# Optimization experiments

Hardware: AMD Instinct MI355X
Metric: run time of the kernel (lower is better)

## Reference

```python
import jax, jax.numpy as jnp
import numpy as np

T, N, L, H, C, V = 64, 1024, 128, 512, 64, 64
S = 1 + 1 + H + (L + 1) + L  # pack layout: a(1), v(1), h(H), a_probs(L+1), p(L)


def setup_inputs() -> dict:
    key = jax.random.key(0)
    ks = jax.random.split(key, 16)

    def w(k, shape, fan):
        return jax.random.normal(k, shape, jnp.float32) / np.sqrt(fan)

    return {
        "condition": jax.random.normal(ks[0], (T, N, C), jnp.float32),
        "rnn_hxs": jnp.zeros((N, S), jnp.float32),  # all-zero => new episode
        "emb": w(ks[3], (V, H), H),
        "W0": w(ks[4], (H, C + H), C + H), "b0": jnp.zeros((H,), jnp.float32),
        "W1": w(ks[5], (H, H), H), "b1": jnp.zeros((H,), jnp.float32),
        "W2": w(ks[6], (H, H), H), "b2": jnp.zeros((H,), jnp.float32),
        "W_ih": w(ks[7], (3 * H, H), H), "b_ih": jnp.zeros((3 * H,), jnp.float32),
        "W_hh": w(ks[8], (3 * H, H), H), "b_hh": jnp.zeros((3 * H,), jnp.float32),
        "Wc": w(ks[9], (1, H), H), "bc": jnp.zeros((1,), jnp.float32),
        "Wa": w(ks[10], (4, H), H), "ba": jnp.zeros((4,), jnp.float32),
        "lines": jax.random.randint(ks[1], (N, L), 0, V),
        "actions": jax.random.randint(ks[2], (T, N), 0, L + 1),
    }


def _forward(condition, rnn_hxs, emb, W0, b0, W1, b1, W2, b2,
             W_ih, W_hh, b_ih, b_hh, Wc, bc, Wa, ba, lines, actions):
    M = emb[lines]  # [N, L, H] line embeddings (memory)
    # parse hidden in RecurrentState field order a(1), v(1), h(H), a_probs(L+1), p(L)
    h0 = rnn_hxs[:, 2:2 + H]
    p0 = rnn_hxs[:, 2 + H + (L + 1):]
    new_ep = jnp.all(rnn_hxs == 0, axis=-1)
    p0 = p0.at[:, 0].set(jnp.where(new_ep, 1.0, p0[:, 0]))

    def step(carry, xs):
        h, p = carry
        cond_t, a_t = xs
        # attention readout over memory
        r = jnp.einsum("nl,nlh->nh", p, M)
        # f: MLP on concat(condition, readout)
        x = jnp.concatenate([cond_t, r], axis=-1)
        x = jax.nn.relu(x @ W0.T + b0)
        x = jax.nn.relu(x @ W1.T + b1)
        x = jax.nn.relu(x @ W2.T + b2)
        # torch GRUCell math
        gi = x @ W_ih.T + b_ih
        gh = h @ W_hh.T + b_hh
        i_r, i_z, i_n = jnp.split(gi, 3, axis=-1)
        h_r, h_z, h_n = jnp.split(gh, 3, axis=-1)
        rg = jax.nn.sigmoid(i_r + h_r)
        z = jax.nn.sigmoid(i_z + h_z)
        n = jnp.tanh(i_n + rg * h_n)
        h = (1.0 - z) * n + z * h
        # actor -> 3 shift weights + no-op gate
        k = h @ Wa.T + ba
        l = jax.nn.softmax(k[:, :3], axis=-1)
        no_op = jax.nn.sigmoid(k[:, 3:4])
        # batch_conv1d: per-sample cross-correlation, kernel 3, padding 2 -> len L+2,
        # fold boundary mass inward, then slice [1:-1] -> len L
        xp = jnp.pad(p, ((0, 0), (2, 2)))
        y = (xp[:, 0:L + 2] * l[:, 0:1]
             + xp[:, 1:L + 3] * l[:, 1:2]
             + xp[:, 2:L + 4] * l[:, 2:3])
        y = y.at[:, 1].add(y[:, 0])
        y = y.at[:, L].add(y[:, L + 1])
        conv_p = y[:, 1:L + 1]
        probs = jnp.concatenate([conv_p * (1.0 - no_op), no_op], axis=-1)
        probs = probs / probs.sum(-1, keepdims=True)
        # pointer update (actions supplied non-negative => no sampling branch)
        new = a_t < L
        a = a_t * new.astype(a_t.dtype)
        newf = new.astype(p.dtype)[:, None]
        p = jax.nn.one_hot(a, L, dtype=p.dtype) * newf + p * (1.0 - newf)
        v = h @ Wc.T + bc
        out = jnp.concatenate(
            [a_t.astype(jnp.float32)[:, None], v, h, probs, p], axis=-1)
        return (h, p), out

    _, hx = jax.lax.scan(step, (h0, p0), (condition, actions))
    return hx  # [T, N, S]


def reference(condition, rnn_hxs, emb, W0, b0, W1, b1, W2, b2,
              W_ih, W_hh, b_ih, b_hh, Wc, bc, Wa, ba, lines, actions):
    hx = _forward(condition, rnn_hxs, emb, W0, b0, W1, b1, W2, b2,
                  W_ih, W_hh, b_ih, b_hh, Wc, bc, Wa, ba, lines, actions)
    return hx, hx[-1:]
```

## Files before the change

kernel.cpp:

```cpp
#include <hip/hip_runtime.h>
#include <hip/hip_bf16.h>
#include <stdint.h>

#define T_ 64
#define N_ 1024
#define L_ 128
#define H_ 512
#define C_ 64
#define S_ 771
#define TN_ (T_*N_)

typedef unsigned short u16;
typedef unsigned int u32;
typedef float f32x4 __attribute__((ext_vector_type(4)));
typedef __bf16 bf16x8 __attribute__((ext_vector_type(8)));
typedef u16 u16x8 __attribute__((ext_vector_type(8)));

#define WAITVM(n) do { asm volatile("s_waitcnt vmcnt(" #n ")" ::: "memory"); \
                       __builtin_amdgcn_sched_barrier(0); } while (0)

__device__ __forceinline__ u16 f2bf(float f) {
  u32 u = __float_as_uint(f);
  u32 r = (u + 0x7FFFu + ((u >> 16) & 1u)) >> 16;
  return (u16)r;
}
__device__ __forceinline__ float bf2f(u16 u) {
  return __uint_as_float(((u32)u) << 16);
}
__device__ __forceinline__ void gload16(const void* g, void* l) {
  __builtin_amdgcn_global_load_lds((const __attribute__((address_space(1))) u32*)g,
                                   (__attribute__((address_space(3))) u32*)l, 16, 0, 0);
}
__device__ __forceinline__ float sigm(float x) { return 1.0f / (1.0f + __expf(-x)); }

__device__ __forceinline__ bf16x8 load_cc(const u16* p) {
  bf16x8 v;
  asm volatile("global_load_dwordx4 %0, %1, off sc0 sc1" : "=v"(v) : "v"(p) : "memory");
  return v;
}
__device__ __forceinline__ void store_cc_d2(u16* p, uint2 val) {
  asm volatile("global_store_dwordx2 %0, %1, off sc0 sc1" :: "v"(p), "v"(val) : "memory");
}
__device__ __forceinline__ float gi_get(uint2 u, int v) {
  u32 w = (v < 2) ? u.x : u.y;
  u16 h = (v & 1) ? (u16)(w >> 16) : (u16)(w & 0xffffu);
  return bf2f(h);
}

__global__ void cast_f32_bf16(const float* __restrict__ src, u16* __restrict__ dst, int n) {
  int i = blockIdx.x * 256 + threadIdx.x;
  if (i < n) dst[i] = f2bf(src[i]);
}

__global__ void qscan(const float* __restrict__ hxs, const int* __restrict__ actions,
                      int* __restrict__ qpre, int* __restrict__ qpost) {
  int n = blockIdx.x * 256 + threadIdx.x;
  if (n >= N_) return;
  bool nz = false;
  for (int s = 0; s < S_; ++s) nz |= (hxs[(size_t)n * S_ + s] != 0.0f);
  int q = 0;
  if (nz) {
    float best = -3.4e38f;
    for (int l = 0; l < L_; ++l) {
      float v = hxs[(size_t)n * S_ + 2 + H_ + (L_ + 1) + l];
      if (v > best) { best = v; q = l; }
    }
  }
  for (int t = 0; t < T_; ++t) {
    qpre[t * N_ + n] = q;
    int a = actions[t * N_ + n];
    if (a < L_) q = a;
    qpost[t * N_ + n] = q;
  }
}

__global__ void hbf_init(const float* __restrict__ hxs, u16* __restrict__ hsave0) {
  int i = blockIdx.x * 256 + threadIdx.x;
  if (i >= N_ * H_) return;
  int n = i >> 9, j = i & 511;
  hsave0[i] = f2bf(hxs[(size_t)n * S_ + 2 + j]);
}

__global__ void build_abuf(const float* __restrict__ cond, const float* __restrict__ emb,
                           const int* __restrict__ lines, const int* __restrict__ qpre,
                           u16* __restrict__ abuf) {
  int row = blockIdx.x * 4 + (threadIdx.x >> 6);
  int lane = threadIdx.x & 63;
  int n = row & (N_ - 1);
  int q = qpre[row];
  int line = lines[n * L_ + q];
  abuf[(size_t)row * 576 + lane] = f2bf(cond[(size_t)row * 64 + lane]);
  const float* er = emb + (size_t)line * H_;
  u16* ar = abuf + (size_t)row * 576 + 64;
  for (int j = lane; j < H_; j += 64) ar[j] = f2bf(er[j]);
}

#define BM 128
#define BN 128
#define BK 64
__global__ __launch_bounds__(256) void gemm_nt(
    const u16* __restrict__ A, int lda,
    const u16* __restrict__ B, int ldb,
    const float* __restrict__ bias,
    u16* __restrict__ C, int ldc,
    int K, int relu)
{
  __shared__ __align__(16) u16 lA[BM * BK];
  __shared__ __align__(16) u16 lB[BN * BK];
  int tid = threadIdx.x;
  int lane = tid & 63;
  int wave = tid >> 6;
  int wm = wave >> 1, wn = wave & 1;
  int m0 = blockIdx.y * BM;
  int n0 = blockIdx.x * BN;

  f32x4 acc[4][4];
  f32x4 zero = {0.f, 0.f, 0.f, 0.f};
#pragma unroll
  for (int i = 0; i < 4; ++i)
#pragma unroll
    for (int j = 0; j < 4; ++j) acc[i][j] = zero;

  int nkt = K / BK;
  for (int kt = 0; kt < nkt; ++kt) {
#pragma unroll
    for (int it = 0; it < 4; ++it) {
      int s = it * 256 + tid;
      int row = s >> 3, cs = s & 7;
      gload16(A + (size_t)(m0 + row) * lda + kt * BK + cs * 8,
              lA + (size_t)(it * 256 + (tid & ~63)) * 8);
      gload16(B + (size_t)(n0 + row) * ldb + kt * BK + cs * 8,
              lB + (size_t)(it * 256 + (tid & ~63)) * 8);
    }
    __syncthreads();
#pragma unroll
    for (int ks = 0; ks < 2; ++ks) {
      bf16x8 af[4], bfr[4];
#pragma unroll
      for (int fm = 0; fm < 4; ++fm) {
        int rowa = wm * 64 + fm * 16 + (lane & 15);
        af[fm] = *(const bf16x8*)&lA[rowa * BK + ks * 32 + ((lane >> 4) << 3)];
      }
#pragma unroll
      for (int fn = 0; fn < 4; ++fn) {
        int rowb = wn * 64 + fn * 16 + (lane & 15);
        bfr[fn] = *(const bf16x8*)&lB[rowb * BK + ks * 32 + ((lane >> 4) << 3)];
      }
#pragma unroll
      for (int fm = 0; fm < 4; ++fm)
#pragma unroll
        for (int fn = 0; fn < 4; ++fn)
          acc[fm][fn] = __builtin_amdgcn_mfma_f32_16x16x32_bf16(af[fm], bfr[fn], acc[fm][fn], 0, 0, 0);
    }
    __syncthreads();
  }
#pragma unroll
  for (int fm = 0; fm < 4; ++fm) {
#pragma unroll
    for (int fn = 0; fn < 4; ++fn) {
      int col = n0 + wn * 64 + fn * 16 + (lane & 15);
      float b = bias[col];
#pragma unroll
      for (int v = 0; v < 4; ++v) {
        int row = m0 + wm * 64 + fm * 16 + ((lane >> 4) << 2) + v;
        float val = acc[fm][fn][v] + b;
        if (relu) val = fmaxf(val, 0.0f);
        C[(size_t)row * ldc + col] = f2bf(val);
      }
    }
  }
}

__global__ __launch_bounds__(256, 1) void gru_persistent(
    const u16* __restrict__ GI,
    const u16* __restrict__ WHH,
    u16* __restrict__ Hsave,
    const float* __restrict__ hxs,
    const float* __restrict__ bhh,
    int* __restrict__ bar)
{
  int tid = threadIdx.x;
  int lane = tid & 63;
  int wave = tid >> 6;
  int wj = wave >> 1, wn = wave & 1;
  int bid = blockIdx.x;
  int mt = bid & 15, jt = bid >> 4;
  int n0 = mt * 64 + wn * 32;
  int jb = jt * 32 + wj * 16;
  int l15 = lane & 15, l4 = lane >> 4;
  int jt4 = l4 * 4;

  bf16x8 afr[3][16];
#pragma unroll
  for (int g = 0; g < 3; ++g) {
    const u16* base = WHH + (size_t)(g * 512 + jb + l15) * 512 + l4 * 8;
#pragma unroll
    for (int kk = 0; kk < 16; ++kk)
      afr[g][kk] = *(const bf16x8*)(base + kk * 32);
  }

  float bb[3][4];
#pragma unroll
  for (int g = 0; g < 3; ++g)
#pragma unroll
    for (int v = 0; v < 4; ++v) bb[g][v] = bhh[g * 512 + jb + jt4 + v];

  float hreg[2][4];
#pragma unroll
  for (int nt = 0; nt < 2; ++nt)
#pragma unroll
    for (int v = 0; v < 4; ++v)
      hreg[nt][v] = hxs[(size_t)(n0 + nt * 16 + l15) * S_ + 2 + jb + jt4 + v];

  for (int t = 0; t < T_; ++t) {
    const u16* Hin = Hsave + (size_t)t * (N_ * 512);
    u16* Hout = Hsave + (size_t)(t + 1) * (N_ * 512);
    const size_t tb = (size_t)t * N_;

    uint2 giu[2][3];
#pragma unroll
    for (int nt = 0; nt < 2; ++nt) {
      const u16* gr = GI + (tb + n0 + nt * 16 + l15) * 1536 + jb + jt4;
#pragma unroll
      for (int g = 0; g < 3; ++g)
        giu[nt][g] = *(const uint2*)(gr + (size_t)g * 512);
    }

    if (t > 0) {
      if (tid == 0) {
        const int* cptr = bar + mt * T_ + (t - 1);
        while (__hip_atomic_load(cptr, __ATOMIC_RELAXED, __HIP_MEMORY_SCOPE_AGENT) < 16)
          __builtin_amdgcn_s_sleep(2);
      }
      __syncthreads();
    }

    f32x4 zero = {0.f, 0.f, 0.f, 0.f};
    f32x4 acc[2][3] = {{zero, zero, zero}, {zero, zero, zero}};

#pragma unroll
    for (int nt = 0; nt < 2; ++nt) {
      bf16x8 areg[16];
      const u16* arow = Hin + (size_t)(n0 + nt * 16 + l15) * 512 + l4 * 8;
#pragma unroll
      for (int kk = 0; kk < 16; ++kk) areg[kk] = load_cc(arow + kk * 32);
      WAITVM(8);
#pragma unroll
      for (int kk = 0; kk < 8; ++kk)
#pragma unroll
        for (int g = 0; g < 3; ++g)
          acc[nt][g] = __builtin_amdgcn_mfma_f32_16x16x32_bf16(afr[g][kk], areg[kk], acc[nt][g], 0, 0, 0);
      WAITVM(0);
#pragma unroll
      for (int kk = 8; kk < 16; ++kk)
#pragma unroll
        for (int g = 0; g < 3; ++g)
          acc[nt][g] = __builtin_amdgcn_mfma_f32_16x16x32_bf16(afr[g][kk], areg[kk], acc[nt][g], 0, 0, 0);
    }

#pragma unroll
    for (int nt = 0; nt < 2; ++nt) {
      int n = n0 + nt * 16 + l15;
      u32 pk0 = 0, pk1 = 0;
#pragma unroll
      for (int v = 0; v < 4; ++v) {
        float r = sigm(gi_get(giu[nt][0], v) + acc[nt][0][v] + bb[0][v]);
        float z = sigm(gi_get(giu[nt][1], v) + acc[nt][1][v] + bb[1][v]);
        float nn = tanhf(gi_get(giu[nt][2], v) + r * (acc[nt][2][v] + bb[2][v]));
        float h = (1.0f - z) * nn + z * hreg[nt][v];
        hreg[nt][v] = h;
        u32 hb = (u32)f2bf(h);
        if (v == 0) pk0 = hb;
        else if (v == 1) pk0 |= hb << 16;
        else if (v == 2) pk1 = hb;
        else pk1 |= hb << 16;
      }
      uint2 pk; pk.x = pk0; pk.y = pk1;
      store_cc_d2(Hout + (size_t)n * 512 + jb + jt4, pk);
    }

    if (t < T_ - 1) {
      WAITVM(0);
      __syncthreads();
      if (tid == 0)
        __hip_atomic_fetch_add(bar + mt * T_ + t, 1, __ATOMIC_RELAXED, __HIP_MEMORY_SCOPE_AGENT);
    }
  }
}

__global__ __launch_bounds__(256) void heads_kernel(
    const u16* __restrict__ Hsave,
    const float* __restrict__ Wc, const float* __restrict__ bc,
    const float* __restrict__ Wa, const float* __restrict__ ba,
    const int* __restrict__ actions, const int* __restrict__ qpre,
    const int* __restrict__ qpost, float* __restrict__ out)
{
  int row = blockIdx.x * 4 + (threadIdx.x >> 6);
  int lane = threadIdx.x & 63;
  const u16x8 hv8 = *(const u16x8*)(Hsave + (size_t)(N_ + row) * 512 + lane * 8);
  float* oh = out + (size_t)row * S_ + 2 + lane * 8;
  float pc = 0, p0 = 0, p1 = 0, p2 = 0, p3 = 0;
#pragma unroll
  for (int jj = 0; jj < 8; ++jj) {
    int k = lane * 8 + jj;
    float hv = bf2f(hv8[jj]);
    oh[jj] = hv;
    pc += hv * Wc[k];
    p0 += hv * Wa[k];
    p1 += hv * Wa[512 + k];
    p2 += hv * Wa[1024 + k];
    p3 += hv * Wa[1536 + k];
  }
#pragma unroll
  for (int m = 1; m < 64; m <<= 1) {
    pc += __shfl_xor(pc, m);
    p0 += __shfl_xor(p0, m);
    p1 += __shfl_xor(p1, m);
    p2 += __shfl_xor(p2, m);
    p3 += __shfl_xor(p3, m);
  }
  float v = pc + bc[0];
  float k0 = p0 + ba[0], k1 = p1 + ba[1], k2 = p2 + ba[2], k3 = p3 + ba[3];
  float mx = fmaxf(k0, fmaxf(k1, k2));
  float e0 = __expf(k0 - mx), e1 = __expf(k1 - mx), e2 = __expf(k2 - mx);
  float es = e0 + e1 + e2;
  float l0 = e0 / es, l1 = e1 / es, l2 = e2 / es;
  float no = sigm(k3);
  float total = (1.0f - no) * (l0 + l1 + l2) + no;
  float sc = (1.0f - no) / total;
  int q = qpre[row], qp = qpost[row];
  int a = actions[row];
  if (lane == 0) {
    out[(size_t)row * S_] = (float)a;
    out[(size_t)row * S_ + 1] = v;
  }
  float* pr = out + (size_t)row * S_ + 2 + H_;
  for (int c = lane; c < L_ + 1; c += 64) {
    float val;
    if (c == L_) val = no / total;
    else {
      val = 0.f;
      if (q == 0)            { if (c == 0) val = l1 + l2; else if (c == 1) val = l0; }
      else if (q == L_ - 1)  { if (c == L_ - 2) val = l2; else if (c == L_ - 1) val = l0 + l1; }
      else                   { if (c == q - 1) val = l2; else if (c == q) val = l1; else if (c == q + 1) val = l0; }
      val *= sc;
    }
    pr[c] = val;
  }
  float* pp = pr + (L_ + 1);
  for (int c = lane; c < L_; c += 64) pp[c] = (c == qp) ? 1.0f : 0.0f;
}

__global__ void copy_last(float* __restrict__ out) {
  int i = blockIdx.x * 256 + threadIdx.x;
  if (i < N_ * S_) out[(size_t)TN_ * S_ + i] = out[(size_t)(T_ - 1) * N_ * S_ + i];
}

extern "C" void kernel_launch(void* const* d_in, const int* in_sizes, int n_in,
                              void* d_out, int out_size, void* d_ws, size_t ws_size,
                              hipStream_t stream) {
  const float* cond = (const float*)d_in[0];
  const float* hxs  = (const float*)d_in[1];
  const float* emb  = (const float*)d_in[2];
  const float* W0   = (const float*)d_in[3];
  const float* b0   = (const float*)d_in[4];
  const float* W1   = (const float*)d_in[5];
  const float* b1   = (const float*)d_in[6];
  const float* W2   = (const float*)d_in[7];
  const float* b2   = (const float*)d_in[8];
  const float* Wih  = (const float*)d_in[9];
  const float* bih  = (const float*)d_in[10];
  const float* Whh  = (const float*)d_in[11];
  const float* bhh  = (const float*)d_in[12];
  const float* Wc   = (const float*)d_in[13];
  const float* bc   = (const float*)d_in[14];
  const float* Wa   = (const float*)d_in[15];
  const float* ba   = (const float*)d_in[16];
  const int* lines   = (const int*)d_in[17];
  const int* actions = (const int*)d_in[18];
  float* out = (float*)d_out;

  char* ws = (char*)d_ws;
  size_t off = 0;
  auto alloc = [&](size_t bytes) {
    char* p = ws + off;
    off += (bytes + 255) & ~(size_t)255;
    return p;
  };
  u16* P = (u16*)alloc((size_t)TN_ * 576 * 2);
  u16* Q = (u16*)alloc((size_t)TN_ * 512 * 2);
  u16* GIb = (u16*)alloc((size_t)TN_ * 1536 * 2);
  u16* Abuf = P;
  u16* X1 = Q;
  u16* X2 = P;
  u16* X3 = Q;
  u16* W0b = (u16*)alloc((size_t)512 * 576 * 2);
  u16* W1b = (u16*)alloc((size_t)512 * 512 * 2);
  u16* W2b = (u16*)alloc((size_t)512 * 512 * 2);
  u16* WIHb = (u16*)alloc((size_t)1536 * 512 * 2);
  u16* WHHb = (u16*)alloc((size_t)1536 * 512 * 2);
  int* qpre  = (int*)alloc((size_t)TN_ * 4);
  int* qpost = (int*)alloc((size_t)TN_ * 4);
  u16* Hsave = (u16*)alloc((size_t)(T_ + 1) * N_ * 512 * 2);
  int* bar = (int*)alloc((size_t)16 * T_ * 4);

  hipMemsetAsync(bar, 0, (size_t)16 * T_ * 4, stream);

  cast_f32_bf16<<<(512 * 576 + 255) / 256, 256, 0, stream>>>(W0, W0b, 512 * 576);
  cast_f32_bf16<<<(512 * 512 + 255) / 256, 256, 0, stream>>>(W1, W1b, 512 * 512);
  cast_f32_bf16<<<(512 * 512 + 255) / 256, 256, 0, stream>>>(W2, W2b, 512 * 512);
  cast_f32_bf16<<<(1536 * 512 + 255) / 256, 256, 0, stream>>>(Wih, WIHb, 1536 * 512);
  cast_f32_bf16<<<(1536 * 512 + 255) / 256, 256, 0, stream>>>(Whh, WHHb, 1536 * 512);
  qscan<<<4, 256, 0, stream>>>(hxs, actions, qpre, qpost);
  hbf_init<<<(N_ * 512 + 255) / 256, 256, 0, stream>>>(hxs, Hsave);
  build_abuf<<<TN_ / 4, 256, 0, stream>>>(cond, emb, lines, qpre, Abuf);

  gemm_nt<<<dim3(4, 512), 256, 0, stream>>>(Abuf, 576, W0b, 576, b0, X1, 512, 576, 1);
  gemm_nt<<<dim3(4, 512), 256, 0, stream>>>(X1, 512, W1b, 512, b1, X2, 512, 512, 1);
  gemm_nt<<<dim3(4, 512), 256, 0, stream>>>(X2, 512, W2b, 512, b2, X3, 512, 512, 1);
  gemm_nt<<<dim3(12, 512), 256, 0, stream>>>(X3, 512, WIHb, 512, bih, GIb, 1536, 512, 0);

  gru_persistent<<<256, 256, 0, stream>>>(GIb, WHHb, Hsave, hxs, bhh, bar);

  heads_kernel<<<TN_ / 4, 256, 0, stream>>>(Hsave, Wc, bc, Wa, ba, actions, qpre, qpost, out);
  copy_last<<<(N_ * S_ + 255) / 256, 256, 0, stream>>>(out);
}
```

Measured before the change: 1.022 ms.

## Replace atomic step barrier with flag array, merge launches, parallelize qscan

Replaces the per-step atomic counter barrier in the persistent GRU kernel with a per-row-group flag array. Each block stores its step number with a cache-coherent store, and the waiter reads all 16 flags in one vector poll. Both H tiles' loads are now issued before any MFMA, with staged waitcnts, and the weight fragments are pinned in registers. Several smaller launches are consolidated: the five weight casts become one kernel, copy_last is folded into heads_kernel, and qscan runs one wave per row instead of one thread per row. The flag barrier relies on the plain stores becoming visible at device scope without atomics.

```diff
diff --git a/kernel.cpp b/kernel.cpp
--- a/kernel.cpp
+++ b/kernel.cpp
@@ -15,9 +15,11 @@
 typedef float f32x4 __attribute__((ext_vector_type(4)));
 typedef __bf16 bf16x8 __attribute__((ext_vector_type(8)));
 typedef u16 u16x8 __attribute__((ext_vector_type(8)));
+typedef u32 u32x4 __attribute__((ext_vector_type(4)));
 
 #define WAITVM(n) do { asm volatile("s_waitcnt vmcnt(" #n ")" ::: "memory"); \
                        __builtin_amdgcn_sched_barrier(0); } while (0)
+#define PIN(x) asm volatile("" : "+v"(x))
 
 __device__ __forceinline__ u16 f2bf(float f) {
   u32 u = __float_as_uint(f);
@@ -38,8 +40,16 @@
   asm volatile("global_load_dwordx4 %0, %1, off sc0 sc1" : "=v"(v) : "v"(p) : "memory");
   return v;
 }
+__device__ __forceinline__ u32x4 load_cc4(const int* p) {
+  u32x4 v;
+  asm volatile("global_load_dwordx4 %0, %1, off sc0 sc1" : "=v"(v) : "v"(p) : "memory");
+  return v;
+}
 __device__ __forceinline__ void store_cc_d2(u16* p, uint2 val) {
   asm volatile("global_store_dwordx2 %0, %1, off sc0 sc1" :: "v"(p), "v"(val) : "memory");
+}
+__device__ __forceinline__ void store_cc_u32(int* p, u32 val) {
+  asm volatile("global_store_dword %0, %1, off sc0 sc1" :: "v"(p), "v"(val) : "memory");
 }
 __device__ __forceinline__ float gi_get(uint2 u, int v) {
   u32 w = (v < 2) ? u.x : u.y;
@@ -47,30 +57,52 @@
   return bf2f(h);
 }
 
-__global__ void cast_f32_bf16(const float* __restrict__ src, u16* __restrict__ dst, int n) {
+#define CA0 294912
+#define CA1 557056
+#define CA2 819200
+#define CA3 1605632
+#define CTOT 2392064
+__global__ void cast_all(const float* __restrict__ W0, const float* __restrict__ W1,
+                         const float* __restrict__ W2, const float* __restrict__ Wih,
+                         const float* __restrict__ Whh, u16* __restrict__ dst) {
   int i = blockIdx.x * 256 + threadIdx.x;
-  if (i < n) dst[i] = f2bf(src[i]);
+  if (i >= CTOT) return;
+  float v;
+  if (i < CA0)      v = W0[i];
+  else if (i < CA1) v = W1[i - CA0];
+  else if (i < CA2) v = W2[i - CA1];
+  else if (i < CA3) v = Wih[i - CA2];
+  else              v = Whh[i - CA3];
+  dst[i] = f2bf(v);
 }
 
 __global__ void qscan(const float* __restrict__ hxs, const int* __restrict__ actions,
                       int* __restrict__ qpre, int* __restrict__ qpost) {
-  int n = blockIdx.x * 256 + threadIdx.x;
-  if (n >= N_) return;
+  int wave = threadIdx.x >> 6, lane = threadIdx.x & 63;
+  int n = blockIdx.x * 4 + wave;
   bool nz = false;
-  for (int s = 0; s < S_; ++s) nz |= (hxs[(size_t)n * S_ + s] != 0.0f);
+  for (int s = lane; s < S_; s += 64) nz |= (hxs[(size_t)n * S_ + s] != 0.0f);
+  unsigned long long bal = __ballot(nz);
   int q = 0;
-  if (nz) {
-    float best = -3.4e38f;
-    for (int l = 0; l < L_; ++l) {
+  if (bal) {
+    float best = -3.4e38f; int bi = L_;
+    for (int l = lane; l < L_; l += 64) {
       float v = hxs[(size_t)n * S_ + 2 + H_ + (L_ + 1) + l];
-      if (v > best) { best = v; q = l; }
-    }
-  }
-  for (int t = 0; t < T_; ++t) {
-    qpre[t * N_ + n] = q;
-    int a = actions[t * N_ + n];
-    if (a < L_) q = a;
-    qpost[t * N_ + n] = q;
+      if (v > best) { best = v; bi = l; }
+    }
+    for (int m = 32; m; m >>= 1) {
+      float ob = __shfl_xor(best, m); int oi = __shfl_xor(bi, m);
+      if (ob > best || (ob == best && oi < bi)) { best = ob; bi = oi; }
+    }
+    q = (bi < L_) ? bi : 0;
+  }
+  if (lane == 0) {
+    for (int t = 0; t < T_; ++t) {
+      qpre[t * N_ + n] = q;
+      int a = actions[t * N_ + n];
+      if (a < L_) q = a;
+      qpost[t * N_ + n] = q;
+    }
   }
 }
 
@@ -198,6 +230,10 @@
     for (int kk = 0; kk < 16; ++kk)
       afr[g][kk] = *(const bf16x8*)(base + kk * 32);
   }
+#pragma unroll
+  for (int g = 0; g < 3; ++g)
+#pragma unroll
+    for (int kk = 0; kk < 16; ++kk) PIN(afr[g][kk]);
 
   float bb[3][4];
 #pragma unroll
@@ -211,6 +247,8 @@
 #pragma unroll
     for (int v = 0; v < 4; ++v)
       hreg[nt][v] = hxs[(size_t)(n0 + nt * 16 + l15) * S_ + 2 + jb + jt4 + v];
+
+  int* bmt = bar + mt * 16;
 
   for (int t = 0; t < T_; ++t) {
     const u16* Hin = Hsave + (size_t)t * (N_ * 512);
@@ -228,35 +266,59 @@
 
     if (t > 0) {
       if (tid == 0) {
-        const int* cptr = bar + mt * T_ + (t - 1);
-        while (__hip_atomic_load(cptr, __ATOMIC_RELAXED, __HIP_MEMORY_SCOPE_AGENT) < 16)
+        for (;;) {
+          u32x4 a = load_cc4(bmt), b = load_cc4(bmt + 4);
+          u32x4 c = load_cc4(bmt + 8), d = load_cc4(bmt + 12);
+          WAITVM(0);
+          u32 m0v = a[0]; 
+#pragma unroll
+          for (int i = 1; i < 4; ++i) m0v = m0v < a[i] ? m0v : a[i];
+#pragma unroll
+          for (int i = 0; i < 4; ++i) { m0v = m0v < b[i] ? m0v : b[i];
+                                        m0v = m0v < c[i] ? m0v : c[i];
+                                        m0v = m0v < d[i] ? m0v : d[i]; }
+          if ((int)m0v >= t) break;
           __builtin_amdgcn_s_sleep(2);
+        }
       }
       __syncthreads();
     }
 
+    bf16x8 areg[2][16];
+#pragma unroll
+    for (int nt = 0; nt < 2; ++nt) {
+      const u16* arow = Hin + (size_t)(n0 + nt * 16 + l15) * 512 + l4 * 8;
+#pragma unroll
+      for (int kk = 0; kk < 16; ++kk) areg[nt][kk] = load_cc(arow + kk * 32);
+    }
+
     f32x4 zero = {0.f, 0.f, 0.f, 0.f};
     f32x4 acc[2][3] = {{zero, zero, zero}, {zero, zero, zero}};
 
-#pragma unroll
-    for (int nt = 0; nt < 2; ++nt) {
-      bf16x8 areg[16];
-      const u16* arow = Hin + (size_t)(n0 + nt * 16 + l15) * 512 + l4 * 8;
-#pragma unroll
-      for (int kk = 0; kk < 16; ++kk) areg[kk] = load_cc(arow + kk * 32);
-      WAITVM(8);
-#pragma unroll
-      for (int kk = 0; kk < 8; ++kk)
-#pragma unroll
-        for (int g = 0; g < 3; ++g)
-          acc[nt][g] = __builtin_amdgcn_mfma_f32_16x16x32_bf16(afr[g][kk], areg[kk], acc[nt][g], 0, 0, 0);
-      WAITVM(0);
-#pragma unroll
-      for (int kk = 8; kk < 16; ++kk)
-#pragma unroll
-        for (int g = 0; g < 3; ++g)
-          acc[nt][g] = __builtin_amdgcn_mfma_f32_16x16x32_bf16(afr[g][kk], areg[kk], acc[nt][g], 0, 0, 0);
-    }
+    WAITVM(24);
+#pragma unroll
+    for (int kk = 0; kk < 8; ++kk)
+#pragma unroll
+      for (int g = 0; g < 3; ++g)
+        acc[0][g] = __builtin_amdgcn_mfma_f32_16x16x32_bf16(afr[g][kk], areg[0][kk], acc[0][g], 0, 0, 0);
+    WAITVM(16);
+#pragma unroll
+    for (int kk = 8; kk < 16; ++kk)
+#pragma unroll
+      for (int g = 0; g < 3; ++g)
+        acc[0][g] = __builtin_amdgcn_mfma_f32_16x16x32_bf16(afr[g][kk], areg[0][kk], acc[0][g], 0, 0, 0);
+    WAITVM(8);
+#pragma unroll
+    for (int kk = 0; kk < 8; ++kk)
+#pragma unroll
+      for (int g = 0; g < 3; ++g)
+        acc[1][g] = __builtin_amdgcn_mfma_f32_16x16x32_bf16(afr[g][kk], areg[1][kk], acc[1][g], 0, 0, 0);
+    WAITVM(0);
+#pragma unroll
+    for (int kk = 8; kk < 16; ++kk)
+#pragma unroll
+      for (int g = 0; g < 3; ++g)
+        acc[1][g] = __builtin_amdgcn_mfma_f32_16x16x32_bf16(afr[g][kk], areg[1][kk], acc[1][g], 0, 0, 0);
 
 #pragma unroll
     for (int nt = 0; nt < 2; ++nt) {
@@ -282,8 +344,7 @@
     if (t < T_ - 1) {
       WAITVM(0);
       __syncthreads();
-      if (tid == 0)
-        __hip_atomic_fetch_add(bar + mt * T_ + t, 1, __ATOMIC_RELAXED, __HIP_MEMORY_SCOPE_AGENT);
+      if (tid == 0) store_cc_u32(bmt + jt, (u32)(t + 1));
     }
   }
 }
@@ -297,6 +358,8 @@
 {
   int row = blockIdx.x * 4 + (threadIdx.x >> 6);
   int lane = threadIdx.x & 63;
+  bool last = row >= (T_ - 1) * N_;
+  const int DUP = N_ * S_;
   const u16x8 hv8 = *(const u16x8*)(Hsave + (size_t)(N_ + row) * 512 + lane * 8);
   float* oh = out + (size_t)row * S_ + 2 + lane * 8;
   float pc = 0, p0 = 0, p1 = 0, p2 = 0, p3 = 0;
@@ -305,6 +368,7 @@
     int k = lane * 8 + jj;
     float hv = bf2f(hv8[jj]);
     oh[jj] = hv;
+    if (last) oh[DUP + jj] = hv;
     pc += hv * Wc[k];
     p0 += hv * Wa[k];
     p1 += hv * Wa[512 + k];
@@ -333,6 +397,10 @@
   if (lane == 0) {
     out[(size_t)row * S_] = (float)a;
     out[(size_t)row * S_ + 1] = v;
+    if (last) {
+      out[(size_t)row * S_ + DUP] = (float)a;
+      out[(size_t)row * S_ + DUP + 1] = v;
+    }
   }
   float* pr = out + (size_t)row * S_ + 2 + H_;
   for (int c = lane; c < L_ + 1; c += 64) {
@@ -346,14 +414,14 @@
       val *= sc;
     }
     pr[c] = val;
+    if (last) pr[DUP + c] = val;
   }
   float* pp = pr + (L_ + 1);
-  for (int c = lane; c < L_; c += 64) pp[c] = (c == qp) ? 1.0f : 0.0f;
-}
-
-__global__ void copy_last(float* __restrict__ out) {
-  int i = blockIdx.x * 256 + threadIdx.x;
-  if (i < N_ * S_) out[(size_t)TN_ * S_ + i] = out[(size_t)(T_ - 1) * N_ * S_ + i];
+  for (int c = lane; c < L_; c += 64) {
+    float val = (c == qp) ? 1.0f : 0.0f;
+    pp[c] = val;
+    if (last) pp[DUP + c] = val;
+  }
 }
 
 extern "C" void kernel_launch(void* const* d_in, const int* in_sizes, int n_in,
@@ -402,16 +470,12 @@
   int* qpre  = (int*)alloc((size_t)TN_ * 4);
   int* qpost = (int*)alloc((size_t)TN_ * 4);
   u16* Hsave = (u16*)alloc((size_t)(T_ + 1) * N_ * 512 * 2);
-  int* bar = (int*)alloc((size_t)16 * T_ * 4);
-
-  hipMemsetAsync(bar, 0, (size_t)16 * T_ * 4, stream);
-
-  cast_f32_bf16<<<(512 * 576 + 255) / 256, 256, 0, stream>>>(W0, W0b, 512 * 576);
-  cast_f32_bf16<<<(512 * 512 + 255) / 256, 256, 0, stream>>>(W1, W1b, 512 * 512);
-  cast_f32_bf16<<<(512 * 512 + 255) / 256, 256, 0, stream>>>(W2, W2b, 512 * 512);
-  cast_f32_bf16<<<(1536 * 512 + 255) / 256, 256, 0, stream>>>(Wih, WIHb, 1536 * 512);
-  cast_f32_bf16<<<(1536 * 512 + 255) / 256, 256, 0, stream>>>(Whh, WHHb, 1536 * 512);
-  qscan<<<4, 256, 0, stream>>>(hxs, actions, qpre, qpost);
+  int* bar = (int*)alloc((size_t)16 * 16 * 4);
+
+  hipMemsetAsync(bar, 0, (size_t)16 * 16 * 4, stream);
+
+  cast_all<<<(CTOT + 255) / 256, 256, 0, stream>>>(W0, W1, W2, Wih, Whh, W0b);
+  qscan<<<256, 256, 0, stream>>>(hxs, actions, qpre, qpost);
   hbf_init<<<(N_ * 512 + 255) / 256, 256, 0, stream>>>(hxs, Hsave);
   build_abuf<<<TN_ / 4, 256, 0, stream>>>(cond, emb, lines, qpre, Abuf);
 
@@ -423,5 +487,4 @@
   gru_persistent<<<256, 256, 0, stream>>>(GIb, WHHb, Hsave, hxs, bhh, bar);
 
   heads_kernel<<<TN_ / 4, 256, 0, stream>>>(Hsave, Wc, bc, Wa, ba, actions, qpre, qpost, out);
-  copy_last<<<(N_ * S_ + 255) / 256, 256, 0, stream>>>(out);
-}
+}
```

After: 1.264 ms. +23.7%, slower.
